# Performance work log

Measured on AMD Instinct MI355X. Metric: run time of the kernel, lower is better.

The kernel has to match this reference:

```python
import jax, jax.numpy as jnp
import numpy as np

DIM = 512
HEADS = 8
DIM_HEAD = 64  # dim // 8
LANDMARKS = 256  # dim // 2
PINV_ITERS = 6
CONV_K = 33  # residual_conv_kernel default in nystrom-attention
SCALE = DIM_HEAD ** -0.5


def setup_inputs() -> dict:
    key = jax.random.key(0)
    ks = jax.random.split(key, 6)
    B, N = 4, 4096
    inner = HEADS * DIM_HEAD  # 512
    x = jax.random.normal(ks[0], (B, N, DIM), dtype=jnp.float32)
    gamma = jnp.ones((DIM,), jnp.float32)
    beta = jnp.zeros((DIM,), jnp.float32)
    w_qkv = jax.random.normal(ks[1], (DIM, 3 * inner), jnp.float32) * 0.02
    w_out = jax.random.normal(ks[2], (inner, DIM), jnp.float32) * 0.02
    b_out = jnp.zeros((DIM,), jnp.float32)
    # depthwise Conv2d(heads, heads, (33,1), groups=heads, bias=False): OIHW = (H,1,33,1)
    conv_w = jax.random.normal(ks[3], (HEADS, 1, CONV_K, 1), jnp.float32) * 0.1
    return {"x": x, "gamma": gamma, "beta": beta, "w_qkv": w_qkv,
            "w_out": w_out, "b_out": b_out, "conv_w": conv_w}


def _layernorm(x, gamma, beta, eps=1e-5):
    mu = x.mean(-1, keepdims=True)
    var = ((x - mu) ** 2).mean(-1, keepdims=True)
    return (x - mu) * jax.lax.rsqrt(var + eps) * gamma + beta


def _pinv_newton_schulz(a, iters=PINV_ITERS):
    # Moore-Penrose pseudo-inverse via iterative scheme (lucidrains)
    abs_a = jnp.abs(a)
    col = abs_a.sum(-1).max()  # global scalar max, as torch.max
    row = abs_a.sum(-2).max()
    z = jnp.swapaxes(a, -1, -2) / (col * row)
    I = jnp.eye(a.shape[-1], dtype=a.dtype)
    for _ in range(iters):
        az = a @ z
        z = 0.25 * z @ (13. * I - az @ (15. * I - az @ (7. * I - az)))
    return z


def reference(x, gamma, beta, w_qkv, w_out, b_out, conv_w):
    B, N, _ = x.shape
    m = LANDMARKS
    l = N // m  # N chosen divisible by m, so no padding branch
    xn = _layernorm(x, gamma, beta)
    qkv = xn @ w_qkv  # [B,N,3*inner]
    q, k, v = jnp.split(qkv, 3, axis=-1)
    # [B,H,N,D]
    def split_heads(t):
        return t.reshape(B, N, HEADS, DIM_HEAD).transpose(0, 2, 1, 3)
    q, k, v = split_heads(q) * SCALE, split_heads(k), split_heads(v)
    # landmarks: mean over contiguous groups of l tokens -> [B,H,m,D]
    q_l = q.reshape(B, HEADS, m, l, DIM_HEAD).mean(3)
    k_l = k.reshape(B, HEADS, m, l, DIM_HEAD).mean(3)
    attn1 = jax.nn.softmax(jnp.einsum('bhid,bhjd->bhij', q, k_l), axis=-1)    # [B,H,N,m]
    attn2 = jax.nn.softmax(jnp.einsum('bhid,bhjd->bhij', q_l, k_l), axis=-1)  # [B,H,m,m]
    attn3 = jax.nn.softmax(jnp.einsum('bhid,bhjd->bhij', q_l, k), axis=-1)    # [B,H,m,N]
    attn2_inv = _pinv_newton_schulz(attn2)
    out = (attn1 @ attn2_inv) @ (attn3 @ v)  # [B,H,N,D]
    # residual depthwise conv over sequence dim, per head (channels=heads)
    out = out + jax.lax.conv_general_dilated(
        v, conv_w, window_strides=(1, 1),
        padding=[(CONV_K // 2, CONV_K // 2), (0, 0)],
        dimension_numbers=('NCHW', 'OIHW', 'NCHW'),
        feature_group_count=HEADS)
    out = out.transpose(0, 2, 1, 3).reshape(B, N, HEADS * DIM_HEAD)
    attn_out = out @ w_out + b_out  # dropout is identity at eval
    return x + attn_out
```

## Files before the change

kernel.cpp:

```cpp
#include <hip/hip_runtime.h>
#include <math.h>

#define BH 32
#define N_ 4096
#define D_ 64
#define M_ 256
#define L_ 16
#define DIM_ 512
#define K3_ 1536

typedef __attribute__((ext_vector_type(4))) float f32x4;
typedef __attribute__((ext_vector_type(8))) short s16x8;
typedef unsigned short ushort_t;

__device__ inline ushort_t f2bf(float f){
  union{float f; unsigned u;} v; v.f = f;
  unsigned r = v.u + 0x7fffu + ((v.u >> 16) & 1u);
  return (ushort_t)(r >> 16);
}
__device__ inline float bf2f(ushort_t b){
  union{unsigned u; float f;} v; v.u = ((unsigned)b) << 16; return v.f;
}

__device__ inline void gl_lds16(const ushort_t* g, ushort_t* l){
  __builtin_amdgcn_global_load_lds(
      (const __attribute__((address_space(1))) unsigned int*)g,
      (__attribute__((address_space(3))) unsigned int*)l, 16, 0, 0);
}

__device__ inline int xcd_swz_bid(){
  int bid = blockIdx.x + gridDim.x*(blockIdx.y + gridDim.y*blockIdx.z);
  int nwg = gridDim.x*gridDim.y*gridDim.z;
  int cpx = nwg >> 3;
  return (bid & 7)*cpx + (bid >> 3);
}

__device__ inline float wave_sum(float v){
  #pragma unroll
  for (int o=32;o;o>>=1) v += __shfl_down(v,o,64);
  return v;
}
__device__ inline float wave_sum_all(float v){
  #pragma unroll
  for (int o=1;o<64;o<<=1) v += __shfl_xor(v,o,64);
  return v;
}
__device__ inline float wave_max(float v){
  #pragma unroll
  for (int o=32;o;o>>=1) v = fmaxf(v,__shfl_down(v,o,64));
  return v;
}
__device__ inline float blk_max256(float v, float* sm){
  v = wave_max(v);
  int lane = threadIdx.x & 63, wid = threadIdx.x >> 6;
  if (lane==0) sm[wid]=v;
  __syncthreads();
  float r = fmaxf(fmaxf(sm[0],sm[1]),fmaxf(sm[2],sm[3]));
  __syncthreads();
  return r;
}

__global__ __launch_bounds__(256) void ln2_k(const float* __restrict__ x,
    const float* __restrict__ g, const float* __restrict__ bt, ushort_t* __restrict__ xn){
  int t = threadIdx.x, lane = t & 63, w = t >> 6;
  size_t row = (size_t)blockIdx.x*4 + w;
  const float* xr = x + row*DIM_;
  f32x4 a = *(const f32x4*)&xr[lane*8];
  f32x4 b = *(const f32x4*)&xr[lane*8+4];
  float s = a[0]+a[1]+a[2]+a[3]+b[0]+b[1]+b[2]+b[3];
  float mu = wave_sum_all(s) * (1.f/DIM_);
  float d[8];
  #pragma unroll
  for (int i=0;i<4;i++){ d[i] = a[i]-mu; d[i+4] = b[i]-mu; }
  float vs = 0.f;
  #pragma unroll
  for (int i=0;i<8;i++) vs += d[i]*d[i];
  float var = wave_sum_all(vs) * (1.f/DIM_);
  float rs = rsqrtf(var + 1e-5f);
  f32x4 g0 = *(const f32x4*)&g[lane*8], g1 = *(const f32x4*)&g[lane*8+4];
  f32x4 b0 = *(const f32x4*)&bt[lane*8], b1 = *(const f32x4*)&bt[lane*8+4];
  ushort_t tmp[8];
  #pragma unroll
  for (int i=0;i<4;i++){
    tmp[i]   = f2bf(d[i]*rs*g0[i]   + b0[i]);
    tmp[i+4] = f2bf(d[i+4]*rs*g1[i] + b1[i]);
  }
  *(uint4*)&xn[row*DIM_ + lane*8] = *(uint4*)tmp;
}

__global__ __launch_bounds__(256) void twb_k(const float* __restrict__ src,
    ushort_t* __restrict__ dst, int R, int C){
  __shared__ ushort_t tile[64][66];
  size_t boff = (size_t)blockIdx.z * R * C;
  int r0 = blockIdx.y*64, c0 = blockIdx.x*64;
  int t = threadIdx.x, c = t & 63, r4 = t >> 6;
  #pragma unroll
  for (int i=0;i<16;i++){
    int rr = r4 + i*4;
    tile[c][rr] = f2bf(src[boff + (size_t)(r0+rr)*C + (c0+c)]);
  }
  __syncthreads();
  #pragma unroll
  for (int i=0;i<16;i++){
    int cc = r4 + i*4;
    dst[boff + (size_t)(c0+cc)*R + (r0 + c)] = tile[cc][c];
  }
}
__global__ __launch_bounds__(256) void tbb_k(const ushort_t* __restrict__ src,
    ushort_t* __restrict__ dst, int R, int C){
  __shared__ ushort_t tile[64][66];
  size_t boff = (size_t)blockIdx.z * R * C;
  int r0 = blockIdx.y*64, c0 = blockIdx.x*64;
  int t = threadIdx.x, c = t & 63, r4 = t >> 6;
  #pragma unroll
  for (int i=0;i<16;i++){
    int rr = r4 + i*4;
    tile[c][rr] = src[boff + (size_t)(r0+rr)*C + (c0+c)];
  }
  __syncthreads();
  #pragma unroll
  for (int i=0;i<16;i++){
    int cc = r4 + i*4;
    dst[boff + (size_t)(c0+cc)*R + (r0 + c)] = tile[cc][c];
  }
}

__global__ __launch_bounds__(256) void gemm_qkv_k(const ushort_t* __restrict__ A,
    const ushort_t* __restrict__ Bt, ushort_t* __restrict__ qb, ushort_t* __restrict__ kb,
    ushort_t* __restrict__ vb){
  __shared__ __align__(16) ushort_t As[128*64];
  __shared__ __align__(16) ushort_t Bs[128*64];
  int t = threadIdx.x;
  int lane = t & 63, wave = t >> 6;
  int l16 = lane & 15, quad = lane >> 4;
  int wm = (wave & 1) * 64, wn = (wave >> 1) * 64;
  int swz = xcd_swz_bid();
  int bx = swz % gridDim.x, by = swz / gridDim.x;
  int row0 = by * 128, col0 = bx * 128;
  f32x4 acc[4][4];
  #pragma unroll
  for (int i=0;i<4;i++)
    #pragma unroll
    for (int j=0;j<4;j++) acc[i][j] = (f32x4){0.f,0.f,0.f,0.f};
  int lr = lane >> 3, lc = lane & 7;
  int scol = (lc ^ lr) * 8;
  int rx7 = l16 & 7;
  for (int k0=0;k0<DIM_;k0+=64){
    __syncthreads();
    #pragma unroll
    for (int p=0;p<4;p++){
      int r = wave*8 + p*32;
      gl_lds16(&A [(size_t)(row0+r+lr)*DIM_ + k0 + scol], &As[(size_t)r*64]);
      gl_lds16(&Bt[(size_t)(col0+r+lr)*DIM_ + k0 + scol], &Bs[(size_t)r*64]);
    }
    __syncthreads();
    s16x8 af[4][2], bf[4][2];
    #pragma unroll
    for (int mt=0;mt<4;mt++)
      #pragma unroll
      for (int kk=0;kk<2;kk++)
        af[mt][kk] = *(const s16x8*)&As[(wm + mt*16 + l16)*64 + (((kk*4+quad)^rx7)*8)];
    #pragma unroll
    for (int nt=0;nt<4;nt++)
      #pragma unroll
      for (int kk=0;kk<2;kk++)
        bf[nt][kk] = *(const s16x8*)&Bs[(wn + nt*16 + l16)*64 + (((kk*4+quad)^rx7)*8)];
    #pragma unroll
    for (int mt=0;mt<4;mt++)
      #pragma unroll
      for (int nt=0;nt<4;nt++)
        #pragma unroll
        for (int kk=0;kk<2;kk++)
          acc[mt][nt] = __builtin_amdgcn_mfma_f32_16x16x32_bf16(af[mt][kk], bf[nt][kk], acc[mt][nt], 0,0,0);
  }
  #pragma unroll
  for (int mt=0;mt<4;mt++){
    #pragma unroll
    for (int nt=0;nt<4;nt++){
      #pragma unroll
      for (int reg=0;reg<4;reg++){
        int row = row0 + wm + mt*16 + quad*4 + reg;
        int col = col0 + wn + nt*16 + l16;
        float val = acc[mt][nt][reg];
        int b = row >> 12, n = row & 4095;
        int which = col >> 9, rem = col & 511;
        int h = rem >> 6, d = rem & 63;
        size_t dst = ((size_t)((b<<3)+h)*N_ + n)*D_ + d;
        if (which==0)      qb[dst] = f2bf(val*0.125f);
        else if (which==1) kb[dst] = f2bf(val);
        else               vb[dst] = f2bf(val);
      }
    }
  }
}

__global__ __launch_bounds__(256) void final3_k(const ushort_t* __restrict__ A,
    const ushort_t* __restrict__ Bt, const float* __restrict__ bo,
    const float* __restrict__ x, float* __restrict__ y){
  __shared__ __align__(16) ushort_t As[128*64];
  __shared__ __align__(16) ushort_t Bs[64*64];
  int t = threadIdx.x;
  int lane = t & 63, wave = t >> 6;
  int l16 = lane & 15, quad = lane >> 4;
  int wm = wave * 32;
  int swz = xcd_swz_bid();
  int bx = swz % gridDim.x, by = swz / gridDim.x;
  int row0 = by * 128, col0 = bx * 64;
  f32x4 acc[2][4];
  #pragma unroll
  for (int i=0;i<2;i++)
    #pragma unroll
    for (int j=0;j<4;j++) acc[i][j] = (f32x4){0.f,0.f,0.f,0.f};
  int lr = lane >> 3, lc = lane & 7;
  int scol = (lc ^ lr) * 8;
  int rx7 = l16 & 7;
  for (int k0=0;k0<DIM_;k0+=64){
    __syncthreads();
    #pragma unroll
    for (int p=0;p<4;p++){
      int r = wave*8 + p*32;
      gl_lds16(&A[(size_t)(row0+r+lr)*DIM_ + k0 + scol], &As[(size_t)r*64]);
    }
    #pragma unroll
    for (int p=0;p<2;p++){
      int r = wave*8 + p*32;
      gl_lds16(&Bt[(size_t)(col0+r+lr)*DIM_ + k0 + scol], &Bs[(size_t)r*64]);
    }
    __syncthreads();
    s16x8 af[2][2], bf[4][2];
    #pragma unroll
    for (int mt=0;mt<2;mt++)
      #pragma unroll
      for (int kk=0;kk<2;kk++)
        af[mt][kk] = *(const s16x8*)&As[(wm + mt*16 + l16)*64 + (((kk*4+quad)^rx7)*8)];
    #pragma unroll
    for (int nt=0;nt<4;nt++)
      #pragma unroll
      for (int kk=0;kk<2;kk++)
        bf[nt][kk] = *(const s16x8*)&Bs[(nt*16 + l16)*64 + (((kk*4+quad)^rx7)*8)];
    #pragma unroll
    for (int mt=0;mt<2;mt++)
      #pragma unroll
      for (int nt=0;nt<4;nt++)
        #pragma unroll
        for (int kk=0;kk<2;kk++)
          acc[mt][nt] = __builtin_amdgcn_mfma_f32_16x16x32_bf16(af[mt][kk], bf[nt][kk], acc[mt][nt], 0,0,0);
  }
  #pragma unroll
  for (int mt=0;mt<2;mt++){
    #pragma unroll
    for (int nt=0;nt<4;nt++){
      int col = col0 + nt*16 + l16;
      #pragma unroll
      for (int reg=0;reg<4;reg++){
        int row = row0 + wm + mt*16 + quad*4 + reg;
        size_t o = (size_t)row*DIM_ + col;
        y[o] = acc[mt][nt][reg] + bo[col] + x[o];
      }
    }
  }
}

__global__ void lmk_k(const ushort_t* __restrict__ q, const ushort_t* __restrict__ k,
                      float* __restrict__ ql, float* __restrict__ kl,
                      ushort_t* __restrict__ qlh, ushort_t* __restrict__ qll,
                      ushort_t* __restrict__ klh, ushort_t* __restrict__ kll){
  int idx = blockIdx.x*256 + threadIdx.x;
  int d = idx & 63, i = (idx >> 6) & 255, bh = idx >> 14;
  size_t base = ((size_t)bh*N_ + i*L_)*D_ + d;
  float sq=0.f, sk=0.f;
  #pragma unroll
  for (int tt=0;tt<L_;tt++){ sq += bf2f(q[base + (size_t)tt*D_]); sk += bf2f(k[base + (size_t)tt*D_]); }
  sq *= (1.f/L_); sk *= (1.f/L_);
  ql[idx] = sq; kl[idx] = sk;
  ushort_t qh = f2bf(sq), kh = f2bf(sk);
  qlh[idx] = qh; qll[idx] = f2bf(sq - bf2f(qh));
  klh[idx] = kh; kll[idx] = f2bf(sk - bf2f(kh));
}

__global__ __launch_bounds__(256) void attn2m_k(
    const ushort_t* __restrict__ qlh, const ushort_t* __restrict__ qll,
    const ushort_t* __restrict__ klh, const ushort_t* __restrict__ kll,
    float* __restrict__ a2f, ushort_t* __restrict__ a2h, ushort_t* __restrict__ a2l,
    float* __restrict__ cs, float* __restrict__ rs){
  int bh = blockIdx.y;
  int t = threadIdx.x, wave = t >> 6, lane = t & 63;
  int l16 = lane & 15, quad = lane >> 4;
  size_t mo = (size_t)bh*M_*M_;
  int rowtile = blockIdx.x*32 + wave*16;
  size_t qbase = ((size_t)bh*M_ + rowtile + l16)*D_;
  s16x8 qh0 = *(const s16x8*)&qlh[qbase + quad*8];
  s16x8 qh1 = *(const s16x8*)&qlh[qbase + 32 + quad*8];
  s16x8 qv0 = *(const s16x8*)&qll[qbase + quad*8];
  s16x8 qv1 = *(const s16x8*)&qll[qbase + 32 + quad*8];
  f32x4 s[16];
  #pragma unroll
  for (int kt=0;kt<16;kt++){
    size_t kb = ((size_t)bh*M_ + kt*16 + l16)*D_;
    s16x8 kh0 = *(const s16x8*)&klh[kb + quad*8];
    s16x8 kh1 = *(const s16x8*)&klh[kb + 32 + quad*8];
    s16x8 kv0 = *(const s16x8*)&kll[kb + quad*8];
    s16x8 kv1 = *(const s16x8*)&kll[kb + 32 + quad*8];
    f32x4 z = (f32x4){0.f,0.f,0.f,0.f};
    z = __builtin_amdgcn_mfma_f32_16x16x32_bf16(qh0, kh0, z, 0,0,0);
    z = __builtin_amdgcn_mfma_f32_16x16x32_bf16(qh1, kh1, z, 0,0,0);
    z = __builtin_amdgcn_mfma_f32_16x16x32_bf16(qh0, kv0, z, 0,0,0);
    z = __builtin_amdgcn_mfma_f32_16x16x32_bf16(qh1, kv1, z, 0,0,0);
    z = __builtin_amdgcn_mfma_f32_16x16x32_bf16(qv0, kh0, z, 0,0,0);
    z = __builtin_amdgcn_mfma_f32_16x16x32_bf16(qv1, kh1, z, 0,0,0);
    s[kt] = z;
  }
  float mx[4], inv[4];
  #pragma unroll
  for (int r=0;r<4;r++){
    float m = s[0][r];
    #pragma unroll
    for (int kt=1;kt<16;kt++) m = fmaxf(m, s[kt][r]);
    m = fmaxf(m, __shfl_xor(m, 1));
    m = fmaxf(m, __shfl_xor(m, 2));
    m = fmaxf(m, __shfl_xor(m, 4));
    m = fmaxf(m, __shfl_xor(m, 8));
    mx[r] = m;
  }
  float lsum[4] = {0.f,0.f,0.f,0.f};
  #pragma unroll
  for (int kt=0;kt<16;kt++){
    #pragma unroll
    for (int r=0;r<4;r++){
      float e = expf(s[kt][r] - mx[r]);
      s[kt][r] = e;
      lsum[r] += e;
    }
  }
  #pragma unroll
  for (int r=0;r<4;r++){
    float ls = lsum[r];
    ls += __shfl_xor(ls, 1);
    ls += __shfl_xor(ls, 2);
    ls += __shfl_xor(ls, 4);
    ls += __shfl_xor(ls, 8);
    inv[r] = 1.f/ls;
  }
  if (l16 == 0){
    #pragma unroll
    for (int r=0;r<4;r++) rs[(size_t)bh*M_ + rowtile + quad*4 + r] = 1.0f;
  }
  #pragma unroll
  for (int kt=0;kt<16;kt++){
    int c = kt*16 + l16;
    float csum = 0.f;
    #pragma unroll
    for (int r=0;r<4;r++){
      float p = s[kt][r]*inv[r];
      csum += p;
      size_t oi = mo + (size_t)(rowtile + quad*4 + r)*M_ + c;
      a2f[oi] = p;
      ushort_t hh = f2bf(p);
      a2h[oi] = hh;
      a2l[oi] = f2bf(p - bf2f(hh));
    }
    csum += __shfl_xor(csum, 16);
    csum += __shfl_xor(csum, 32);
    if (lane < 16) atomicAdd(&cs[(size_t)bh*M_ + c], csum);
  }
}

__global__ __launch_bounds__(256) void maxred_k(const float* __restrict__ cs,
    const float* __restrict__ rs, float* __restrict__ scal){
  __shared__ float sm[4];
  float cm=-1e30f, rm=-1e30f;
  for (int i=threadIdx.x;i<BH*M_;i+=256){ cm=fmaxf(cm,cs[i]); rm=fmaxf(rm,rs[i]); }
  cm = blk_max256(cm, sm);
  rm = blk_max256(rm, sm);
  if (threadIdx.x==0) scal[0] = 1.f/(cm*rm);
}

__global__ __launch_bounds__(256) void initz3_k(const float* __restrict__ a2,
    const float* __restrict__ scal,
    ushort_t* __restrict__ zh, ushort_t* __restrict__ zl,
    ushort_t* __restrict__ zTh, ushort_t* __restrict__ zTl){
  __shared__ float tile[64][65];
  int bh = blockIdx.z;
  size_t mo = (size_t)bh*M_*M_;
  float s = scal[0];
  int r0 = blockIdx.y*64, c0 = blockIdx.x*64;
  int t = threadIdx.x, c = t & 63, r4 = t >> 6;
  #pragma unroll
  for (int i=0;i<16;i++){
    int rr = r4 + i*4;
    float v = a2[mo + (size_t)(r0+rr)*M_ + c0 + c] * s;
    tile[rr][c] = v;
    ushort_t hh = f2bf(v);
    size_t oi = mo + (size_t)(r0+rr)*M_ + c0 + c;
    zTh[oi] = hh;
    zTl[oi] = f2bf(v - bf2f(hh));
  }
  __syncthreads();
  #pragma unroll
  for (int i=0;i<16;i++){
    int zr = r4 + i*4;
    float v = tile[c][zr];
    size_t oi = mo + (size_t)(c0+zr)*M_ + r0 + c;
    ushort_t hh = f2bf(v);
    zh[oi] = hh;
    zl[oi] = f2bf(v - bf2f(hh));
  }
}

template<bool HASCOEF, bool WN, bool WT, bool WF>
__global__ __launch_bounds__(256) void ns3_k(
    const ushort_t* __restrict__ Ah, const ushort_t* __restrict__ Al,
    const ushort_t* __restrict__ BTh, const ushort_t* __restrict__ BTl,
    float coef, float scale,
    ushort_t* __restrict__ Ch, ushort_t* __restrict__ Cl,
    ushort_t* __restrict__ CTh, ushort_t* __restrict__ CTl,
    float* __restrict__ Cf){
  __shared__ __align__(16) ushort_t Ahs[64*64];
  __shared__ __align__(16) ushort_t Als[64*64];
  __shared__ __align__(16) ushort_t Bhs[64*64];
  __shared__ __align__(16) ushort_t Bls[64*64];
  int swz = xcd_swz_bid();
  int bx = swz % gridDim.x; int rem = swz / gridDim.x;
  int by = rem % gridDim.y; int batch = rem / gridDim.y;
  size_t mo = (size_t)batch*M_*M_;
  int row0 = by*64, col0 = bx*64;
  int t = threadIdx.x, lane = t & 63, wave = t >> 6;
  int l16 = lane & 15, quad = lane >> 4;
  f32x4 acc[4];
  #pragma unroll
  for (int j=0;j<4;j++) acc[j] = (f32x4){0.f,0.f,0.f,0.f};
  int lr = lane >> 3, lc = lane & 7;
  int scol = (lc ^ lr) * 8;
  int rx7 = l16 & 7;
  for (int k0=0;k0<M_;k0+=64){
    __syncthreads();
    #pragma unroll
    for (int p=0;p<2;p++){
      int r = wave*8 + p*32;
      gl_lds16(&Ah [mo + (size_t)(row0+r+lr)*M_ + k0 + scol], &Ahs[(size_t)r*64]);
      gl_lds16(&Al [mo + (size_t)(row0+r+lr)*M_ + k0 + scol], &Als[(size_t)r*64]);
      gl_lds16(&BTh[mo + (size_t)(col0+r+lr)*M_ + k0 + scol], &Bhs[(size_t)r*64]);
      gl_lds16(&BTl[mo + (size_t)(col0+r+lr)*M_ + k0 + scol], &Bls[(size_t)r*64]);
    }
    __syncthreads();
    s16x8 fah[2], fal[2];
    #pragma unroll
    for (int kk=0;kk<2;kk++){
      fah[kk] = *(const s16x8*)&Ahs[(wave*16 + l16)*64 + (((kk*4+quad)^rx7)*8)];
      fal[kk] = *(const s16x8*)&Als[(wave*16 + l16)*64 + (((kk*4+quad)^rx7)*8)];
    }
    #pragma unroll
    for (int nt=0;nt<4;nt++){
      #pragma unroll
      for (int kk=0;kk<2;kk++){
        s16x8 fbh = *(const s16x8*)&Bhs[(nt*16 + l16)*64 + (((kk*4+quad)^rx7)*8)];
        s16x8 fbl = *(const s16x8*)&Bls[(nt*16 + l16)*64 + (((kk*4+quad)^rx7)*8)];
        acc[nt] = __builtin_amdgcn_mfma_f32_16x16x32_bf16(fah[kk], fbh, acc[nt], 0,0,0);
        acc[nt] = __builtin_amdgcn_mfma_f32_16x16x32_bf16(fah[kk], fbl, acc[nt], 0,0,0);
        acc[nt] = __builtin_amdgcn_mfma_f32_16x16x32_bf16(fal[kk], fbh, acc[nt], 0,0,0);
      }
    }
  }
  int rbase = row0 + wave*16 + quad*4;
  #pragma unroll
  for (int nt=0;nt<4;nt++){
    int c = col0 + nt*16 + l16;
    ushort_t th[4], tl[4];
    #pragma unroll
    for (int reg=0;reg<4;reg++){
      float a = acc[nt][reg];
      float base = 0.f;
      if (HASCOEF){
        size_t ai = mo + (size_t)(rbase+reg)*M_ + c;
        base = coef*(bf2f(Ah[ai]) + bf2f(Al[ai]));
      }
      float v = scale*(base - a);
      if (WF) Cf[mo + (size_t)(rbase+reg)*M_ + c] = v;
      ushort_t hh = f2bf(v);
      ushort_t ll = f2bf(v - bf2f(hh));
      if (WN){
        Ch[mo + (size_t)(rbase+reg)*M_ + c] = hh;
        Cl[mo + (size_t)(rbase+reg)*M_ + c] = ll;
      }
      th[reg] = hh; tl[reg] = ll;
    }
    if (WT){
      uint2 vh; vh.x = (unsigned)th[0] | ((unsigned)th[1]<<16); vh.y = (unsigned)th[2] | ((unsigned)th[3]<<16);
      uint2 vl; vl.x = (unsigned)tl[0] | ((unsigned)tl[1]<<16); vl.y = (unsigned)tl[2] | ((unsigned)tl[3]<<16);
      *(uint2*)&CTh[mo + (size_t)c*M_ + rbase] = vh;
      *(uint2*)&CTl[mo + (size_t)c*M_ + rbase] = vl;
    }
  }
}

template<int ITERS, bool SCATTER>
__global__ __launch_bounds__(256) void attn8_k(const ushort_t* __restrict__ Q,
    const ushort_t* __restrict__ K, const ushort_t* __restrict__ VT,
    int nq, int nk,
    float* __restrict__ up, float* __restrict__ mst, float* __restrict__ lst,
    ushort_t* __restrict__ ob){
  __shared__ __align__(16) ushort_t Ks[64*64];
  __shared__ __align__(16) ushort_t Vs[64*64];
  __shared__ __align__(16) ushort_t Pb[4*16*76];
  int swz = xcd_swz_bid();
  int qblk = swz % gridDim.x; int rem0 = swz / gridDim.x;
  int half = rem0 % gridDim.y; int bh = rem0 / gridDim.y;
  int key0 = half * (ITERS*64);
  int t = threadIdx.x, wave = t >> 6, lane = t & 63;
  int l16 = lane & 15, quad = lane >> 4;
  size_t qbase = ((size_t)bh*nq + qblk*64 + wave*16 + l16)*D_;
  s16x8 qa0 = *(const s16x8*)&Q[qbase + quad*8];
  s16x8 qa1 = *(const s16x8*)&Q[qbase + 32 + quad*8];
  const ushort_t* Kb = K + (size_t)bh*nk*D_;
  const ushort_t* Vb = VT + (size_t)bh*D_*nk;
  ushort_t* Pw = &Pb[wave*16*76];
  int lr = lane >> 3, lc = lane & 7;
  int scol = (lc ^ lr) * 8;
  int rx7 = l16 & 7;
  float m_j = -1e30f, l_j = 0.f;
  f32x4 oacc[4];
  #pragma unroll
  for (int d=0;d<4;d++) oacc[d] = (f32x4){0.f,0.f,0.f,0.f};
  for (int it=0; it<ITERS; it++){
    int j0 = key0 + it*64;
    __syncthreads();
    #pragma unroll
    for (int p=0;p<2;p++){
      int r = wave*8 + p*32;
      gl_lds16(&Kb[(size_t)(j0+r+lr)*D_ + scol], &Ks[(size_t)r*64]);
      gl_lds16(&Vb[(size_t)(r+lr)*nk + j0 + scol], &Vs[(size_t)r*64]);
    }
    __syncthreads();
    f32x4 st[4];
    #pragma unroll
    for (int kt=0;kt<4;kt++){
      s16x8 b0 = *(const s16x8*)&Ks[(kt*16 + l16)*64 + ((quad^rx7)*8)];
      s16x8 b1 = *(const s16x8*)&Ks[(kt*16 + l16)*64 + (((4+quad)^rx7)*8)];
      f32x4 z = (f32x4){0.f,0.f,0.f,0.f};
      z = __builtin_amdgcn_mfma_f32_16x16x32_bf16(b0, qa0, z, 0,0,0);
      z = __builtin_amdgcn_mfma_f32_16x16x32_bf16(b1, qa1, z, 0,0,0);
      st[kt] = z;
    }
    float mx = st[0][0];
    #pragma unroll
    for (int kt=0;kt<4;kt++)
      #pragma unroll
      for (int r=0;r<4;r++) mx = fmaxf(mx, st[kt][r]);
    mx = fmaxf(mx, __shfl_xor(mx, 16));
    mx = fmaxf(mx, __shfl_xor(mx, 32));
    float mn = fmaxf(m_j, mx);
    float alpha = __expf(m_j - mn);
    m_j = mn;
    float lsum = 0.f;
    #pragma unroll
    for (int kt=0;kt<4;kt++){
      ushort_t pk[4];
      #pragma unroll
      for (int r=0;r<4;r++){
        float p = __expf(st[kt][r] - mn);
        lsum += p;
        pk[r] = f2bf(p);
      }
      uint2 w;
      w.x = (unsigned)pk[0] | ((unsigned)pk[1] << 16);
      w.y = (unsigned)pk[2] | ((unsigned)pk[3] << 16);
      *(uint2*)&Pw[l16*76 + kt*16 + quad*4] = w;
    }
    lsum += __shfl_xor(lsum, 16);
    lsum += __shfl_xor(lsum, 32);
    l_j = l_j*alpha + lsum;
    float ab[4];
    #pragma unroll
    for (int r=0;r<4;r++) ab[r] = __shfl(alpha, quad*4 + r, 64);
    #pragma unroll
    for (int d=0;d<4;d++)
      #pragma unroll
      for (int r=0;r<4;r++) oacc[d][r] *= ab[r];
    #pragma unroll
    for (int ks=0;ks<2;ks++){
      s16x8 pa = *(const s16x8*)&Pw[l16*76 + ks*32 + quad*8];
      #pragma unroll
      for (int dt=0;dt<4;dt++){
        s16x8 vv = *(const s16x8*)&Vs[(dt*16 + l16)*64 + (((ks*4+quad)^rx7)*8)];
        oacc[dt] = __builtin_amdgcn_mfma_f32_16x16x32_bf16(pa, vv, oacc[dt], 0,0,0);
      }
    }
  }
  int rowbase = qblk*64 + wave*16 + quad*4;
  if (SCATTER){
    float lb[4];
    #pragma unroll
    for (int r=0;r<4;r++) lb[r] = __shfl(l_j, quad*4 + r, 64);
    int b = bh >> 3, h = bh & 7;
    #pragma unroll
    for (int dt=0;dt<4;dt++){
      #pragma unroll
      for (int r=0;r<4;r++){
        int n = rowbase + r;
        ob[((size_t)(b*N_ + n))*DIM_ + h*D_ + dt*16 + l16] = f2bf(oacc[dt][r] / lb[r]);
      }
    }
  } else {
    size_t pb = ((size_t)(half*BH + bh)*M_ + rowbase)*D_;
    #pragma unroll
    for (int dt=0;dt<4;dt++){
      #pragma unroll
      for (int r=0;r<4;r++)
        up[pb + (size_t)r*D_ + dt*16 + l16] = oacc[dt][r];
    }
    if (lane < 16){
      size_t si = (size_t)(half*BH + bh)*M_ + qblk*64 + wave*16 + l16;
      mst[si] = m_j;
      lst[si] = l_j;
    }
  }
}

__global__ __launch_bounds__(256) void comb_k(const float* __restrict__ up,
    const float* __restrict__ mst, const float* __restrict__ lst,
    float* __restrict__ u){
  int idx = blockIdx.x*256 + threadIdx.x;
  int d = idx & 63; int row = (idx >> 6) & 255; int bh = idx >> 14;
  float m = -1e30f;
  float mv[8];
  #pragma unroll
  for (int hfs=0;hfs<8;hfs++){
    mv[hfs] = mst[(size_t)(hfs*BH + bh)*M_ + row];
    m = fmaxf(m, mv[hfs]);
  }
  float num = 0.f, den = 0.f;
  #pragma unroll
  for (int hfs=0;hfs<8;hfs++){
    float w = __expf(mv[hfs] - m);
    size_t ri = (size_t)(hfs*BH + bh)*M_ + row;
    den += lst[ri] * w;
    num += up[ri*D_ + d] * w;
  }
  u[idx] = num / den;
}

__global__ void zu_k(const float* __restrict__ z, const float* __restrict__ u,
                     float* __restrict__ w){
  int idx = blockIdx.x*256 + threadIdx.x;
  int d = idx & 63, i = (idx >> 6) & 255, bh = idx >> 14;
  const float* zr = z + ((size_t)bh*M_+i)*M_;
  const float* ub = u + (size_t)bh*M_*D_ + d;
  float acc = 0.f;
  for (int kk=0;kk<M_;kk++) acc += zr[kk]*ub[(size_t)kk*D_];
  w[idx] = acc;
}

__global__ __launch_bounds__(256) void conv3_k(const ushort_t* __restrict__ v,
    const float* __restrict__ cw, ushort_t* __restrict__ ob){
  int bh = blockIdx.y;
  int h = bh & 7, b = bh >> 3;
  int t = threadIdx.x;
  int d8 = (t & 7) * 8;
  int nloc = t >> 3;
  int n0 = blockIdx.x * 128 + nloc * 4;
  __shared__ float wsm[33];
  if (t < 33) wsm[t] = cw[h*33 + t];
  __syncthreads();
  float acc[4][8];
  #pragma unroll
  for (int j=0;j<4;j++)
    #pragma unroll
    for (int dd=0;dd<8;dd++) acc[j][dd] = 0.f;
  const ushort_t* vbase = v + (size_t)bh*N_*D_;
  for (int r=0;r<36;r++){
    int nn = n0 - 16 + r;
    float vals[8];
    if (nn >= 0 && nn < N_){
      uint4 raw = *(const uint4*)&vbase[(size_t)nn*D_ + d8];
      const ushort_t* pr = (const ushort_t*)&raw;
      #pragma unroll
      for (int dd=0;dd<8;dd++) vals[dd] = bf2f(pr[dd]);
    } else {
      #pragma unroll
      for (int dd=0;dd<8;dd++) vals[dd] = 0.f;
    }
    #pragma unroll
    for (int j=0;j<4;j++){
      int tap = r - j;
      if (tap >= 0 && tap <= 32){
        float wj = wsm[tap];
        #pragma unroll
        for (int dd=0;dd<8;dd++) acc[j][dd] += wj * vals[dd];
      }
    }
  }
  #pragma unroll
  for (int j=0;j<4;j++){
    size_t oi = ((size_t)(b*N_ + n0 + j))*DIM_ + h*D_ + d8;
    uint4 cur = *(uint4*)&ob[oi];
    ushort_t* pc = (ushort_t*)&cur;
    #pragma unroll
    for (int dd=0;dd<8;dd++) pc[dd] = f2bf(bf2f(pc[dd]) + acc[j][dd]);
    *(uint4*)&ob[oi] = cur;
  }
}

extern "C" void kernel_launch(void* const* d_in, const int* in_sizes, int n_in,
                              void* d_out, int out_size, void* d_ws, size_t ws_size,
                              hipStream_t stream){
  (void)in_sizes; (void)n_in; (void)out_size; (void)ws_size;
  const float* x      = (const float*)d_in[0];
  const float* gamma  = (const float*)d_in[1];
  const float* beta   = (const float*)d_in[2];
  const float* w_qkv  = (const float*)d_in[3];
  const float* w_out  = (const float*)d_in[4];
  const float* b_out  = (const float*)d_in[5];
  const float* conv_w = (const float*)d_in[6];
  float* y = (float*)d_out;
  float* ws = (float*)d_ws;

  size_t off = 0;
  ushort_t* xnb   = (ushort_t*)(ws + off); off += 4194304;
  ushort_t* qb    = (ushort_t*)(ws + off); off += 4194304;
  ushort_t* kb    = (ushort_t*)(ws + off); off += 4194304;
  ushort_t* vb    = (ushort_t*)(ws + off); off += 4194304;
  ushort_t* vT    = (ushort_t*)(ws + off); off += 4194304;
  ushort_t* wqkvT = (ushort_t*)(ws + off); off += 393216;
  ushort_t* woutT = (ushort_t*)(ws + off); off += 131072;
  ushort_t* qlh   = (ushort_t*)(ws + off); off += 262144;
  ushort_t* qll   = (ushort_t*)(ws + off); off += 262144;
  ushort_t* klh   = (ushort_t*)(ws + off); off += 262144;
  ushort_t* kll   = (ushort_t*)(ws + off); off += 262144;
  ushort_t* wzT   = (ushort_t*)(ws + off); off += 262144;
  ushort_t* ob    = (ushort_t*)(ws + off); off += 4194304;
  ushort_t* a2h   = (ushort_t*)(ws + off); off += 1048576;
  ushort_t* a2l   = (ushort_t*)(ws + off); off += 1048576;
  ushort_t* z0h   = (ushort_t*)(ws + off); off += 1048576;
  ushort_t* z0l   = (ushort_t*)(ws + off); off += 1048576;
  ushort_t* z0Th  = (ushort_t*)(ws + off); off += 1048576;
  ushort_t* z0Tl  = (ushort_t*)(ws + off); off += 1048576;
  ushort_t* z1h   = (ushort_t*)(ws + off); off += 1048576;
  ushort_t* z1l   = (ushort_t*)(ws + off); off += 1048576;
  ushort_t* z1Th  = (ushort_t*)(ws + off); off += 1048576;
  ushort_t* z1Tl  = (ushort_t*)(ws + off); off += 1048576;
  ushort_t* t1Th  = (ushort_t*)(ws + off); off += 1048576;
  ushort_t* t1Tl  = (ushort_t*)(ws + off); off += 1048576;
  ushort_t* t2Th  = (ushort_t*)(ws + off); off += 1048576;
  ushort_t* t2Tl  = (ushort_t*)(ws + off); off += 1048576;
  float* ql  = ws + off;  off += 524288;
  float* kl  = ws + off;  off += 524288;
  float* a2f = ws + off;  off += 2097152;
  float* zf  = ws + off;  off += 2097152;
  float* u   = ws + off;  off += 524288;
  float* wz  = ws + off;  off += 524288;
  float* up  = ws + off;  off += 4194304;
  float* mstat = ws + off; off += 65536;
  float* lstat = ws + off; off += 65536;
  float* cs  = ws + off;  off += 8192;
  float* rs  = ws + off;  off += 8192;
  float* scal = ws + off; off += 8;
  ushort_t* azh  = xnb;
  ushort_t* azl  = xnb + 2097152;
  ushort_t* azTh = xnb + 2*2097152;
  ushort_t* azTl = xnb + 3*2097152;

  hipMemsetAsync(cs, 0, BH*M_*sizeof(float), stream);
  ln2_k<<<4096,256,0,stream>>>(x, gamma, beta, xnb);
  twb_k<<<dim3(24,8,1),256,0,stream>>>(w_qkv, wqkvT, 512, 1536);
  twb_k<<<dim3(8,8,1),256,0,stream>>>(w_out, woutT, 512, 512);
  gemm_qkv_k<<<dim3(12,128),256,0,stream>>>(xnb, wqkvT, qb, kb, vb);
  tbb_k<<<dim3(1,64,32),256,0,stream>>>(vb, vT, 4096, 64);
  lmk_k<<<2048,256,0,stream>>>(qb, kb, ql, kl, qlh, qll, klh, kll);
  attn2m_k<<<dim3(8,32),128,0,stream>>>(qlh, qll, klh, kll, a2f, a2h, a2l, cs, rs);
  maxred_k<<<1,256,0,stream>>>(cs, rs, scal);
  initz3_k<<<dim3(4,4,32),256,0,stream>>>(a2f, scal, z0h, z0l, z0Th, z0Tl);

  ushort_t *zch = z0h, *zcl = z0l, *zcTh = z0Th, *zcTl = z0Tl;
  ushort_t *znh = z1h, *znl = z1l, *znTh = z1Th, *znTl = z1Tl;
  dim3 nsg(4,4,32);
  for (int it=0; it<6; it++){
    ns3_k<false,true,true,false><<<nsg,256,0,stream>>>(a2h, a2l, zcTh, zcTl,
        0.f, -1.f, azh, azl, azTh, azTl, (float*)nullptr);
    ns3_k<true,false,true,false><<<nsg,256,0,stream>>>(azh, azl, azTh, azTl,
        7.f, 1.f, (ushort_t*)nullptr, (ushort_t*)nullptr, t1Th, t1Tl, (float*)nullptr);
    ns3_k<true,false,true,false><<<nsg,256,0,stream>>>(azh, azl, t1Th, t1Tl,
        15.f, 1.f, (ushort_t*)nullptr, (ushort_t*)nullptr, t2Th, t2Tl, (float*)nullptr);
    if (it < 5)
      ns3_k<true,true,true,false><<<nsg,256,0,stream>>>(zch, zcl, t2Th, t2Tl,
          13.f, 0.25f, znh, znl, znTh, znTl, (float*)nullptr);
    else
      ns3_k<true,true,true,true><<<nsg,256,0,stream>>>(zch, zcl, t2Th, t2Tl,
          13.f, 0.25f, znh, znl, znTh, znTl, zf);
    { ushort_t* tp;
      tp=zch; zch=znh; znh=tp;  tp=zcl; zcl=znl; znl=tp;
      tp=zcTh; zcTh=znTh; znTh=tp;  tp=zcTl; zcTl=znTl; znTl=tp; }
  }

  attn8_k<8,false><<<dim3(4,8,32),256,0,stream>>>(qlh, kb, vT, M_, N_,
      up, mstat, lstat, (ushort_t*)nullptr);
  comb_k<<<2048,256,0,stream>>>(up, mstat, lstat, u);
  zu_k<<<2048,256,0,stream>>>(zf, u, wz);
  twb_k<<<dim3(1,4,32),256,0,stream>>>(wz, wzT, 256, 64);
  attn8_k<4,true><<<dim3(64,1,32),256,0,stream>>>(qb, klh, wzT, N_, M_,
      (float*)nullptr, (float*)nullptr, (float*)nullptr, ob);
  conv3_k<<<dim3(32,32),256,0,stream>>>(vb, conv_w, ob);
  final3_k<<<dim3(8,128),256,0,stream>>>(ob, woutT, b_out, x, y);
}
```

Before: 543.5 us.

## Merge weight transposes, fold max-reduction into init kernel, double attn3 split-K

The two weight-transpose launches become one kernel that picks its source by block index. The separate max-reduction launch is removed: the row-sum max is dropped because softmax rows sum to one, and each initz block recomputes the column-sum max itself. The attn3@v split-K stage now uses 16 splits of 4 tiles instead of 8 of 8, for more parallelism, with comb_k merging 16 partials. In exchange, every initz block redundantly scans 8192 floats, and the partial buffers and combine work grow.

```diff
diff --git a/kernel.cpp b/kernel.cpp
--- a/kernel.cpp
+++ b/kernel.cpp
@@ -35,11 +35,6 @@
   return (bid & 7)*cpx + (bid >> 3);
 }
 
-__device__ inline float wave_sum(float v){
-  #pragma unroll
-  for (int o=32;o;o>>=1) v += __shfl_down(v,o,64);
-  return v;
-}
 __device__ inline float wave_sum_all(float v){
   #pragma unroll
   for (int o=1;o<64;o<<=1) v += __shfl_xor(v,o,64);
@@ -88,6 +83,28 @@
   *(uint4*)&xn[row*DIM_ + lane*8] = *(uint4*)tmp;
 }
 
+__global__ __launch_bounds__(256) void twbw_k(const float* __restrict__ wqkv,
+    ushort_t* __restrict__ wqkvT, const float* __restrict__ wout,
+    ushort_t* __restrict__ woutT){
+  __shared__ ushort_t tile[64][66];
+  const float* src; ushort_t* dst; int R = 512, C;
+  int bx = blockIdx.x;
+  if (bx < 24){ src = wqkv; dst = wqkvT; C = 1536; }
+  else        { src = wout; dst = woutT; C = 512; bx -= 24; }
+  int r0 = blockIdx.y*64, c0 = bx*64;
+  int t = threadIdx.x, c = t & 63, r4 = t >> 6;
+  #pragma unroll
+  for (int i=0;i<16;i++){
+    int rr = r4 + i*4;
+    tile[c][rr] = f2bf(src[(size_t)(r0+rr)*C + (c0+c)]);
+  }
+  __syncthreads();
+  #pragma unroll
+  for (int i=0;i<16;i++){
+    int cc = r4 + i*4;
+    dst[(size_t)(c0+cc)*R + (r0 + c)] = tile[cc][c];
+  }
+}
 __global__ __launch_bounds__(256) void twb_k(const float* __restrict__ src,
     ushort_t* __restrict__ dst, int R, int C){
   __shared__ ushort_t tile[64][66];
@@ -282,7 +299,7 @@
     const ushort_t* __restrict__ qlh, const ushort_t* __restrict__ qll,
     const ushort_t* __restrict__ klh, const ushort_t* __restrict__ kll,
     float* __restrict__ a2f, ushort_t* __restrict__ a2h, ushort_t* __restrict__ a2l,
-    float* __restrict__ cs, float* __restrict__ rs){
+    float* __restrict__ cs){
   int bh = blockIdx.y;
   int t = threadIdx.x, wave = t >> 6, lane = t & 63;
   int l16 = lane & 15, quad = lane >> 4;
@@ -341,10 +358,6 @@
     ls += __shfl_xor(ls, 8);
     inv[r] = 1.f/ls;
   }
-  if (l16 == 0){
-    #pragma unroll
-    for (int r=0;r<4;r++) rs[(size_t)bh*M_ + rowtile + quad*4 + r] = 1.0f;
-  }
   #pragma unroll
   for (int kt=0;kt<16;kt++){
     int c = kt*16 + l16;
@@ -365,24 +378,18 @@
   }
 }
 
-__global__ __launch_bounds__(256) void maxred_k(const float* __restrict__ cs,
-    const float* __restrict__ rs, float* __restrict__ scal){
-  __shared__ float sm[4];
-  float cm=-1e30f, rm=-1e30f;
-  for (int i=threadIdx.x;i<BH*M_;i+=256){ cm=fmaxf(cm,cs[i]); rm=fmaxf(rm,rs[i]); }
-  cm = blk_max256(cm, sm);
-  rm = blk_max256(rm, sm);
-  if (threadIdx.x==0) scal[0] = 1.f/(cm*rm);
-}
-
-__global__ __launch_bounds__(256) void initz3_k(const float* __restrict__ a2,
-    const float* __restrict__ scal,
+__global__ __launch_bounds__(256) void initz4_k(const float* __restrict__ a2,
+    const float* __restrict__ cs,
     ushort_t* __restrict__ zh, ushort_t* __restrict__ zl,
     ushort_t* __restrict__ zTh, ushort_t* __restrict__ zTl){
   __shared__ float tile[64][65];
+  __shared__ float sm[4];
+  float cm = -1e30f;
+  for (int i=threadIdx.x; i<BH*M_; i+=256) cm = fmaxf(cm, cs[i]);
+  cm = blk_max256(cm, sm);
+  float s = 1.f/cm;
   int bh = blockIdx.z;
   size_t mo = (size_t)bh*M_*M_;
-  float s = scal[0];
   int r0 = blockIdx.y*64, c0 = blockIdx.x*64;
   int t = threadIdx.x, c = t & 63, r4 = t >> 6;
   #pragma unroll
@@ -622,15 +629,15 @@
   int idx = blockIdx.x*256 + threadIdx.x;
   int d = idx & 63; int row = (idx >> 6) & 255; int bh = idx >> 14;
   float m = -1e30f;
-  float mv[8];
-  #pragma unroll
-  for (int hfs=0;hfs<8;hfs++){
+  float mv[16];
+  #pragma unroll
+  for (int hfs=0;hfs<16;hfs++){
     mv[hfs] = mst[(size_t)(hfs*BH + bh)*M_ + row];
     m = fmaxf(m, mv[hfs]);
   }
   float num = 0.f, den = 0.f;
   #pragma unroll
-  for (int hfs=0;hfs<8;hfs++){
+  for (int hfs=0;hfs<16;hfs++){
     float w = __expf(mv[hfs] - m);
     size_t ri = (size_t)(hfs*BH + bh)*M_ + row;
     den += lst[ri] * w;
@@ -748,12 +755,10 @@
   float* zf  = ws + off;  off += 2097152;
   float* u   = ws + off;  off += 524288;
   float* wz  = ws + off;  off += 524288;
-  float* up  = ws + off;  off += 4194304;
-  float* mstat = ws + off; off += 65536;
-  float* lstat = ws + off; off += 65536;
+  float* up  = ws + off;  off += 8388608;
+  float* mstat = ws + off; off += 131072;
+  float* lstat = ws + off; off += 131072;
   float* cs  = ws + off;  off += 8192;
-  float* rs  = ws + off;  off += 8192;
-  float* scal = ws + off; off += 8;
   ushort_t* azh  = xnb;
   ushort_t* azl  = xnb + 2097152;
   ushort_t* azTh = xnb + 2*2097152;
@@ -761,14 +766,12 @@
 
   hipMemsetAsync(cs, 0, BH*M_*sizeof(float), stream);
   ln2_k<<<4096,256,0,stream>>>(x, gamma, beta, xnb);
-  twb_k<<<dim3(24,8,1),256,0,stream>>>(w_qkv, wqkvT, 512, 1536);
-  twb_k<<<dim3(8,8,1),256,0,stream>>>(w_out, woutT, 512, 512);
+  twbw_k<<<dim3(32,8,1),256,0,stream>>>(w_qkv, wqkvT, w_out, woutT);
   gemm_qkv_k<<<dim3(12,128),256,0,stream>>>(xnb, wqkvT, qb, kb, vb);
   tbb_k<<<dim3(1,64,32),256,0,stream>>>(vb, vT, 4096, 64);
   lmk_k<<<2048,256,0,stream>>>(qb, kb, ql, kl, qlh, qll, klh, kll);
-  attn2m_k<<<dim3(8,32),128,0,stream>>>(qlh, qll, klh, kll, a2f, a2h, a2l, cs, rs);
-  maxred_k<<<1,256,0,stream>>>(cs, rs, scal);
-  initz3_k<<<dim3(4,4,32),256,0,stream>>>(a2f, scal, z0h, z0l, z0Th, z0Tl);
+  attn2m_k<<<dim3(8,32),128,0,stream>>>(qlh, qll, klh, kll, a2f, a2h, a2l, cs);
+  initz4_k<<<dim3(4,4,32),256,0,stream>>>(a2f, cs, z0h, z0l, z0Th, z0Tl);
 
   ushort_t *zch = z0h, *zcl = z0l, *zcTh = z0Th, *zcTl = z0Tl;
   ushort_t *znh = z1h, *znl = z1l, *znTh = z1Th, *znTl = z1Tl;
@@ -791,7 +794,7 @@
       tp=zcTh; zcTh=znTh; znTh=tp;  tp=zcTl; zcTl=znTl; znTl=tp; }
   }
 
-  attn8_k<8,false><<<dim3(4,8,32),256,0,stream>>>(qlh, kb, vT, M_, N_,
+  attn8_k<4,false><<<dim3(4,16,32),256,0,stream>>>(qlh, kb, vT, M_, N_,
       up, mstat, lstat, (ushort_t*)nullptr);
   comb_k<<<2048,256,0,stream>>>(up, mstat, lstat, u);
   zu_k<<<2048,256,0,stream>>>(zf, u, wz);
```

Result: no change. 537.7 us (-1.1%).
